# Kernel tuning notes

Hardware: AMD Instinct MI355X
Metric: run time of the kernel (lower is better)

## Reference

```python
import jax, jax.numpy as jnp
import numpy as np

B, S, D = 8, 2048, 512
EPS = 1e-6
ROPE_THETA = 10000.0


def setup_inputs() -> dict:
    key = jax.random.key(0)
    ks = jax.random.split(key, 8)
    scale = 0.02
    return {
        "x": jax.random.normal(ks[0], (B, S, D), dtype=jnp.float32),
        "conv_w": jax.random.normal(ks[1], (D, D, 3), dtype=jnp.float32) * scale,
        "conv_b": jnp.zeros((D,), dtype=jnp.float32),
        "pre_g": jnp.ones((D,), dtype=jnp.float32),
        "q_g": jnp.ones((D,), dtype=jnp.float32),
        "k_g": jnp.ones((D,), dtype=jnp.float32),
        "Wq": jax.random.normal(ks[2], (D, D), dtype=jnp.float32) * scale,
        "Wk": jax.random.normal(ks[3], (D, D), dtype=jnp.float32) * scale,
        "Wv": jax.random.normal(ks[4], (D, D), dtype=jnp.float32) * scale,
    }


def _rmsnorm(x, g, eps=EPS):
    ms = jnp.mean(jnp.square(x), axis=-1, keepdims=True)
    return x * jax.lax.rsqrt(ms + eps) * g


def _rope_tables(seq_len, head_dim, dtype=jnp.float32):
    inv = 1.0 / (ROPE_THETA ** (jnp.arange(0, head_dim, 2, dtype=dtype) / head_dim))
    freqs = jnp.arange(seq_len, dtype=dtype)[:, None] * inv[None, :]  # [S, D/2]
    return jnp.cos(freqs), jnp.sin(freqs)


def _apply_rope(x, cos, sin):
    # x: [B, S, D]; treat last dim as D/2 complex pairs (interleaved real/imag)
    b, s, d = x.shape
    xr = x.reshape(b, s, d // 2, 2)
    x0, x1 = xr[..., 0], xr[..., 1]
    c = cos[None, :, :]
    sn = sin[None, :, :]
    o0 = x0 * c - x1 * sn
    o1 = x0 * sn + x1 * c
    return jnp.stack([o0, o1], axis=-1).reshape(b, s, d)


def reference(x, conv_w, conv_b, pre_g, q_g, k_g, Wq, Wk, Wv):
    b, s, d = x.shape
    # Conv1d over sequence axis (kernel 3, padding 1)
    xc = jnp.transpose(x, (0, 2, 1))  # [B, D, S]
    xc = jax.lax.conv_general_dilated(
        xc, conv_w, window_strides=(1,), padding=[(1, 1)],
        dimension_numbers=("NCH", "OIH", "NCH"))
    xc = xc + conv_b[None, :, None]
    x_norm = _rmsnorm(jnp.transpose(xc, (0, 2, 1)), pre_g)  # [B, S, D]

    q = _rmsnorm(jnp.einsum("bsd,ed->bse", x_norm, Wq), q_g)
    k = _rmsnorm(jnp.einsum("bsd,ed->bse", x_norm, Wk), k_g)
    v = jnp.einsum("bsd,ed->bse", x_norm, Wv)

    cos, sin = _rope_tables(s, d, x.dtype)
    q = _apply_rope(q, cos, sin)
    k = _apply_rope(k, cos, sin)

    scores = jnp.einsum("bqd,bkd->bqk", q, k) / jnp.sqrt(jnp.asarray(d, x.dtype))
    w = jax.nn.softmax(scores, axis=-1)  # dropout is identity in eval mode
    attended = jnp.einsum("bqk,bkd->bqd", w, v)
    out = x + attended
    return out.mean(axis=1)  # [B, D]
```

## Files before the change

### kernel.cpp

```cpp
#include <hip/hip_runtime.h>
#include <math.h>

#define BB 8
#define SS 2048
#define SSG 2050
#define DDIM 512
#define KC 1536
#define EPSV 1e-6f
#define SCALE 0.044194173824159216f

typedef unsigned short ushort_t;
using short8 = __attribute__((ext_vector_type(8))) short;
using f32x4  = __attribute__((ext_vector_type(4))) float;

__device__ inline unsigned short f2bf(float f) {
    union { float f; unsigned int u; } v; v.f = f;
    unsigned int r = v.u + 0x7FFFu + ((v.u >> 16) & 1u);
    return (unsigned short)(r >> 16);
}
__device__ inline unsigned int packbf(float a, float b) {
    return (unsigned int)f2bf(a) | ((unsigned int)f2bf(b) << 16);
}
__device__ inline float bf2f(unsigned short s) {
    union { unsigned int u; float f; } v; v.u = ((unsigned int)s) << 16; return v.f;
}

__device__ inline void gload16(const ushort_t* g, ushort_t* l) {
    __builtin_amdgcn_global_load_lds(
        (__attribute__((address_space(1))) const void*)g,
        (__attribute__((address_space(3))) void*)l, 16, 0, 0);
}

__device__ inline short8 ldswz(const ushort_t* s, int row, int c) {
    return *reinterpret_cast<const short8*>(&s[(row << 6) + ((c ^ (row & 7)) << 3)]);
}

__device__ inline ushort_t* crow_ptr(ushort_t* As, ushort_t* Bs, int row) {
    return row < 64 ? As + row * 128 : Bs + (row - 64) * 128;
}

__global__ __launch_bounds__(256) void kx_cast(const float* __restrict__ x,
                                               ushort_t* __restrict__ xbf,
                                               float* __restrict__ xsum)
{
    const int t = threadIdx.x;
    const int b = blockIdx.y;
    const int r0 = blockIdx.x * 16;
    const int c0 = 2 * t;
    if (blockIdx.x == 0) {
        *reinterpret_cast<unsigned int*>(&xbf[((size_t)b * SSG) * DDIM + c0]) = 0u;
        *reinterpret_cast<unsigned int*>(&xbf[((size_t)b * SSG + SS + 1) * DDIM + c0]) = 0u;
    }
    float s0 = 0.f, s1 = 0.f;
    for (int r = 0; r < 16; r++) {
        size_t srow = (size_t)b * SS + r0 + r;
        size_t drow = (size_t)b * SSG + 1 + r0 + r;
        float2 v = *reinterpret_cast<const float2*>(&x[srow * DDIM + c0]);
        s0 += v.x; s1 += v.y;
        *reinterpret_cast<unsigned int*>(&xbf[drow * DDIM + c0]) = packbf(v.x, v.y);
    }
    atomicAdd(&xsum[b * DDIM + c0], s0);
    atomicAdd(&xsum[b * DDIM + c0 + 1], s1);
}

__global__ __launch_bounds__(256) void k0_prep(
    const float* __restrict__ conv_w, const float* __restrict__ Wq,
    const float* __restrict__ Wk, const float* __restrict__ Wv,
    ushort_t* __restrict__ wcat, ushort_t* __restrict__ wqkv)
{
    int idx = blockIdx.x * 256 + threadIdx.x;
    {
        int o = idx / KC, kk = idx - o * KC;
        int t = kk >> 9, i = kk & 511;
        wcat[idx] = f2bf(conv_w[(size_t)o * KC + i * 3 + t]);
    }
    {
        int n = idx >> 9, d = idx & 511;
        const float* src = (n < 512) ? &Wq[(size_t)n * DDIM + d]
                         : (n < 1024) ? &Wk[(size_t)(n - 512) * DDIM + d]
                         : &Wv[(size_t)(n - 1024) * DDIM + d];
        wqkv[idx] = f2bf(*src);
    }
}

__global__ __launch_bounds__(256) void ktab(float* __restrict__ rope)
{
    const int t = threadIdx.x;
    const int r0 = blockIdx.x * 8;
    const float invf = (float)pow(10000.0, -(double)(2 * t) / (double)DDIM);
    for (int r = 0; r < 8; r++) {
        int srow = r0 + r;
        float sn, cs;
        sincosf((float)srow * invf, &sn, &cs);
        *reinterpret_cast<float2*>(&rope[((size_t)srow << 9) + 2 * t]) = make_float2(cs, sn);
    }
}

#define COMPUTE_TILE(Acur, Bcur) do { \
    _Pragma("unroll") \
    for (int half = 0; half < 2; half++) { \
        const int cb = (half << 2) | lq; \
        short8 af0 = ldswz(Acur, wm * 64 +  0 + lm, cb); \
        short8 af1 = ldswz(Acur, wm * 64 + 16 + lm, cb); \
        short8 af2 = ldswz(Acur, wm * 64 + 32 + lm, cb); \
        short8 af3 = ldswz(Acur, wm * 64 + 48 + lm, cb); \
        _Pragma("unroll") \
        for (int nt = 0; nt < 4; nt++) { \
            short8 bfv = ldswz(Bcur, wn * 64 + nt * 16 + lm, cb); \
            acc[0][nt] = __builtin_amdgcn_mfma_f32_16x16x32_bf16(af0, bfv, acc[0][nt], 0, 0, 0); \
            acc[1][nt] = __builtin_amdgcn_mfma_f32_16x16x32_bf16(af1, bfv, acc[1][nt], 0, 0, 0); \
            acc[2][nt] = __builtin_amdgcn_mfma_f32_16x16x32_bf16(af2, bfv, acc[2][nt], 0, 0, 0); \
            acc[3][nt] = __builtin_amdgcn_mfma_f32_16x16x32_bf16(af3, bfv, acc[3][nt], 0, 0, 0); \
        } \
    } } while (0)

#define CSTORE_WIDE(GDSTROW, GPITCH) do { \
    const int row_l = t >> 1, half_ = t & 1, r7_ = row_l & 7; \
    const ushort_t* src_ = crow_ptr(As, Bs, row_l); \
    ushort_t* gdst_ = (GDSTROW); \
    _Pragma("unroll") \
    for (int i = 0; i < 8; i++) { \
        const int j = half_ * 8 + i; \
        *reinterpret_cast<short8*>(&gdst_[j * 8]) = \
            *reinterpret_cast<const short8*>(&src_[(j ^ r7_) << 3]); \
    } } while (0)

__global__ __launch_bounds__(256) void k1b_conv(
    const ushort_t* __restrict__ xbf, const ushort_t* __restrict__ wcat,
    const float* __restrict__ conv_b, ushort_t* __restrict__ ybf, float* __restrict__ rs)
{
    __shared__ alignas(16) ushort_t As[128 * 64];
    __shared__ alignas(16) ushort_t Bs[128 * 64];
    const int t = threadIdx.x;
    const int lane = t & 63, w = t >> 6;
    const int lm = lane & 15, lq = lane >> 4;
    const int wm = w >> 1, wn = w & 1;
    const int lr = lane >> 3;
    const int lc = ((lane & 7) ^ lr) << 3;
    const int s0 = blockIdx.x * 128;
    const int n0 = blockIdx.y * 128;
    const int b  = blockIdx.z;
    const ushort_t* Ag = xbf + (size_t)b * SSG * DDIM;
    const ushort_t* Bg = wcat + (size_t)n0 * KC;

    const ushort_t* pa[4]; const ushort_t* pb[4];
    int la[4];
    #pragma unroll
    for (int i = 0; i < 4; i++) {
        const int tr = (w * 4 + i) * 8 + lr;
        pa[i] = &Ag[(size_t)(s0 + tr) * DDIM + lc];
        pb[i] = &Bg[(size_t)tr * KC + lc];
        la[i] = (w * 4 + i) * 512;
    }

    f32x4 acc[4][4];
    #pragma unroll
    for (int i = 0; i < 4; i++)
        #pragma unroll
        for (int j = 0; j < 4; j++) acc[i][j] = (f32x4){0.f, 0.f, 0.f, 0.f};

    for (int dc = 0; dc < 24; dc++) {
        __syncthreads();
        const int koff = dc * 64;
        #pragma unroll
        for (int i = 0; i < 4; i++) {
            gload16(pa[i] + koff, &As[la[i]]);
            gload16(pb[i] + koff, &Bs[la[i]]);
        }
        __syncthreads();
        COMPUTE_TILE(As, Bs);
    }

    const int rbase = s0 + wm * 64;
    const int cbase = n0 + wn * 64;
    float* rsb = rs + (size_t)b * SS;
    float bias[4];
    #pragma unroll
    for (int nt = 0; nt < 4; nt++) bias[nt] = conv_b[cbase + nt * 16 + lm];
    __syncthreads();
    #pragma unroll
    for (int mt = 0; mt < 4; mt++) {
        #pragma unroll
        for (int r = 0; r < 4; r++) {
            const int rl = wm * 64 + mt * 16 + lq * 4 + r;
            ushort_t* lr_p = crow_ptr(As, Bs, rl);
            const int r7 = rl & 7;
            float pr = 0.f;
            #pragma unroll
            for (int nt = 0; nt < 4; nt++) {
                float val = acc[mt][nt][r] + bias[nt];
                const int c = wn * 64 + nt * 16 + lm;
                lr_p[(((c >> 3) ^ r7) << 3) | (c & 7)] = f2bf(val);
                pr = fmaf(val, val, pr);
            }
            pr += __shfl_xor(pr, 1, 64); pr += __shfl_xor(pr, 2, 64);
            pr += __shfl_xor(pr, 4, 64); pr += __shfl_xor(pr, 8, 64);
            if (lm == 0) atomicAdd(&rsb[rbase + mt * 16 + lq * 4 + r], pr);
        }
    }
    __syncthreads();
    ushort_t* yb = ybf + (size_t)b * SS * DDIM;
    CSTORE_WIDE(&yb[(size_t)(s0 + (t >> 1)) * DDIM + n0], DDIM);
}

__global__ __launch_bounds__(256) void k1n_norm(
    const ushort_t* __restrict__ ybf, const float* __restrict__ rs,
    const float* __restrict__ pre_g, ushort_t* __restrict__ xnbf)
{
    const int t = threadIdx.x;
    const int b = blockIdx.y;
    const int r0 = blockIdx.x * 8;
    float2 pg = *reinterpret_cast<const float2*>(&pre_g[2 * t]);
    for (int r = 0; r < 8; r++) {
        size_t row = (size_t)b * SS + r0 + r;
        float inv = rsqrtf(rs[row] * (1.0f / DDIM) + EPSV);
        unsigned int yv = *reinterpret_cast<const unsigned int*>(&ybf[row * DDIM + 2 * t]);
        float v0 = bf2f((ushort_t)(yv & 0xFFFF)), v1 = bf2f((ushort_t)(yv >> 16));
        *reinterpret_cast<unsigned int*>(&xnbf[row * DDIM + 2 * t]) =
            packbf(v0 * inv * pg.x, v1 * inv * pg.y);
    }
}

__global__ __launch_bounds__(256) void k1c_qkv(
    const ushort_t* __restrict__ xnbf, const ushort_t* __restrict__ wqkv,
    ushort_t* __restrict__ qraw, ushort_t* __restrict__ kraw, ushort_t* __restrict__ vb,
    float* __restrict__ rq, float* __restrict__ rk)
{
    __shared__ alignas(16) ushort_t As[128 * 64];
    __shared__ alignas(16) ushort_t Bs[128 * 64];
    const int t = threadIdx.x;
    const int lane = t & 63, w = t >> 6;
    const int lm = lane & 15, lq = lane >> 4;
    const int wm = w >> 1, wn = w & 1;
    const int lr = lane >> 3;
    const int lc = ((lane & 7) ^ lr) << 3;
    const int s0 = blockIdx.x * 128;
    const int n0 = blockIdx.y * 128;
    const int b  = blockIdx.z;
    const ushort_t* Ag = xnbf + ((size_t)b * SS + s0) * DDIM;
    const ushort_t* Bg = wqkv + (size_t)n0 * DDIM;

    const ushort_t* pa[4]; const ushort_t* pb[4];
    int la[4];
    #pragma unroll
    for (int i = 0; i < 4; i++) {
        const int tr = (w * 4 + i) * 8 + lr;
        pa[i] = &Ag[(size_t)tr * DDIM + lc];
        pb[i] = &Bg[(size_t)tr * DDIM + lc];
        la[i] = (w * 4 + i) * 512;
    }

    f32x4 acc[4][4];
    #pragma unroll
    for (int i = 0; i < 4; i++)
        #pragma unroll
        for (int j = 0; j < 4; j++) acc[i][j] = (f32x4){0.f, 0.f, 0.f, 0.f};

    for (int dc = 0; dc < 8; dc++) {
        __syncthreads();
        const int koff = dc * 64;
        #pragma unroll
        for (int i = 0; i < 4; i++) {
            gload16(pa[i] + koff, &As[la[i]]);
            gload16(pb[i] + koff, &Bs[la[i]]);
        }
        __syncthreads();
        COMPUTE_TILE(As, Bs);
    }

    const int which = blockIdx.y >> 2;
    const int rbase = s0 + wm * 64;
    const int gc0   = (blockIdx.y & 3) * 128;
    __syncthreads();
    if (which == 2) {
        #pragma unroll
        for (int mt = 0; mt < 4; mt++) {
            #pragma unroll
            for (int r = 0; r < 4; r++) {
                const int rl = wm * 64 + mt * 16 + lq * 4 + r;
                ushort_t* lr_p = crow_ptr(As, Bs, rl);
                const int r7 = rl & 7;
                #pragma unroll
                for (int nt = 0; nt < 4; nt++) {
                    const int c = wn * 64 + nt * 16 + lm;
                    lr_p[(((c >> 3) ^ r7) << 3) | (c & 7)] = f2bf(acc[mt][nt][r]);
                }
            }
        }
        __syncthreads();
        ushort_t* vbb = vb + (size_t)b * SS * DDIM;
        CSTORE_WIDE(&vbb[(size_t)(s0 + (t >> 1)) * DDIM + gc0], DDIM);
    } else {
        float* rb = (which ? rk : rq) + (size_t)b * SS;
        #pragma unroll
        for (int mt = 0; mt < 4; mt++) {
            #pragma unroll
            for (int r = 0; r < 4; r++) {
                const int rl = wm * 64 + mt * 16 + lq * 4 + r;
                ushort_t* lr_p = crow_ptr(As, Bs, rl);
                const int r7 = rl & 7;
                float pr = 0.f;
                #pragma unroll
                for (int nt = 0; nt < 4; nt++) {
                    float val = acc[mt][nt][r];
                    const int c = wn * 64 + nt * 16 + lm;
                    lr_p[(((c >> 3) ^ r7) << 3) | (c & 7)] = f2bf(val);
                    pr = fmaf(val, val, pr);
                }
                pr += __shfl_xor(pr, 1, 64); pr += __shfl_xor(pr, 2, 64);
                pr += __shfl_xor(pr, 4, 64); pr += __shfl_xor(pr, 8, 64);
                if (lm == 0) atomicAdd(&rb[rbase + mt * 16 + lq * 4 + r], pr);
            }
        }
        __syncthreads();
        ushort_t* db2 = (which ? kraw : qraw) + (size_t)b * SS * DDIM;
        CSTORE_WIDE(&db2[(size_t)(s0 + (t >> 1)) * DDIM + gc0], DDIM);
    }
}

__global__ __launch_bounds__(256) void k1d_rope(
    ushort_t* q_io, ushort_t* k_io,
    const float* __restrict__ rq, const float* __restrict__ rk,
    const float* __restrict__ q_g, const float* __restrict__ k_g,
    const float* __restrict__ rope)
{
    const int t = threadIdx.x;
    const int b = blockIdx.y;
    const int r0 = blockIdx.x * 8;
    const int c0 = 2 * t;
    float qg0 = q_g[c0], qg1 = q_g[c0 + 1];
    float kg0 = k_g[c0], kg1 = k_g[c0 + 1];
    for (int r = 0; r < 8; r++) {
        int srow = r0 + r;
        size_t rowi = (size_t)b * SS + srow;
        float iq = rsqrtf(rq[rowi] * (1.0f / DDIM) + EPSV);
        float ik = rsqrtf(rk[rowi] * (1.0f / DDIM) + EPSV);
        size_t off = rowi * DDIM + c0;
        unsigned int qv = *reinterpret_cast<const unsigned int*>(&q_io[off]);
        unsigned int kv = *reinterpret_cast<const unsigned int*>(&k_io[off]);
        float q0 = bf2f((ushort_t)(qv & 0xFFFF)) * iq * qg0;
        float q1 = bf2f((ushort_t)(qv >> 16)) * iq * qg1;
        float k0v = bf2f((ushort_t)(kv & 0xFFFF)) * ik * kg0;
        float k1v = bf2f((ushort_t)(kv >> 16)) * ik * kg1;
        float2 cs2 = *reinterpret_cast<const float2*>(&rope[((size_t)srow << 9) + c0]);
        float cs = cs2.x, sn = cs2.y;
        *reinterpret_cast<unsigned int*>(&q_io[off]) = packbf(q0 * cs - q1 * sn, q0 * sn + q1 * cs);
        *reinterpret_cast<unsigned int*>(&k_io[off]) = packbf(k0v * cs - k1v * sn, k0v * sn + k1v * cs);
    }
}

__global__ __launch_bounds__(256) void k2a_rowsum(
    const ushort_t* __restrict__ qb, const ushort_t* __restrict__ kb,
    ushort_t* __restrict__ P, float* __restrict__ l)
{
    __shared__ alignas(16) ushort_t As[128 * 64];
    __shared__ alignas(16) ushort_t Bs[128 * 64];
    const int t = threadIdx.x;
    const int lane = t & 63, w = t >> 6;
    const int lm = lane & 15, lq = lane >> 4;
    const int wm = w >> 1, wn = w & 1;
    const int lr = lane >> 3;
    const int lc = ((lane & 7) ^ lr) << 3;
    const int b  = blockIdx.x;
    const int qt = blockIdx.y;
    const int kt = blockIdx.z;
    const ushort_t* Ag = qb + ((size_t)b * SS + qt * 128) * DDIM;
    const ushort_t* Bg = kb + ((size_t)b * SS + kt * 128) * DDIM;

    const ushort_t* pa[4]; const ushort_t* pb[4];
    int la[4];
    #pragma unroll
    for (int i = 0; i < 4; i++) {
        const int tr = (w * 4 + i) * 8 + lr;
        pa[i] = &Ag[(size_t)tr * DDIM + lc];
        pb[i] = &Bg[(size_t)tr * DDIM + lc];
        la[i] = (w * 4 + i) * 512;
    }

    f32x4 acc[4][4];
    #pragma unroll
    for (int i = 0; i < 4; i++)
        #pragma unroll
        for (int j = 0; j < 4; j++) acc[i][j] = (f32x4){0.f, 0.f, 0.f, 0.f};

    for (int dc = 0; dc < 8; dc++) {
        __syncthreads();
        const int koff = dc * 64;
        #pragma unroll
        for (int i = 0; i < 4; i++) {
            gload16(pa[i] + koff, &As[la[i]]);
            gload16(pb[i] + koff, &Bs[la[i]]);
        }
        __syncthreads();
        COMPUTE_TILE(As, Bs);
    }

    float* lrow = l + (size_t)b * SS + qt * 128;
    __syncthreads();
    #pragma unroll
    for (int mt = 0; mt < 4; mt++) {
        #pragma unroll
        for (int r = 0; r < 4; r++) {
            const int rl = wm * 64 + mt * 16 + lq * 4 + r;
            ushort_t* lr_p = crow_ptr(As, Bs, rl);
            const int r7 = rl & 7;
            float rowp = 0.f;
            #pragma unroll
            for (int nt = 0; nt < 4; nt++) {
                float e = __expf(acc[mt][nt][r] * SCALE);
                const int c = wn * 64 + nt * 16 + lm;
                lr_p[(((c >> 3) ^ r7) << 3) | (c & 7)] = f2bf(e);
                rowp += e;
            }
            rowp += __shfl_xor(rowp, 1, 64); rowp += __shfl_xor(rowp, 2, 64);
            rowp += __shfl_xor(rowp, 4, 64); rowp += __shfl_xor(rowp, 8, 64);
            if (lm == 0) atomicAdd(&lrow[rl], rowp);
        }
    }
    __syncthreads();
    ushort_t* Pb = P + (size_t)b * SS * SS;
    CSTORE_WIDE(&Pb[(size_t)(qt * 128 + (t >> 1)) * SS + kt * 128], SS);
}

__global__ __launch_bounds__(256) void k2c_colred(
    const ushort_t* __restrict__ P, const float* __restrict__ l,
    float* __restrict__ cw)
{
    const int t = threadIdx.x;
    const int b = blockIdx.z;
    const int k0 = blockIdx.x * 1024 + t * 4;
    const int q0 = blockIdx.y * 128;
    const ushort_t* Pb = P + ((size_t)b * SS + q0) * SS;
    const float* lb = l + (size_t)b * SS + q0;
    float a0 = 0.f, a1 = 0.f, a2 = 0.f, a3 = 0.f;
    for (int q = 0; q < 128; q++) {
        float rl = 1.0f / lb[q];
        uint2 pp = *reinterpret_cast<const uint2*>(&Pb[(size_t)q * SS + k0]);
        a0 = fmaf(bf2f((ushort_t)(pp.x & 0xFFFF)), rl, a0);
        a1 = fmaf(bf2f((ushort_t)(pp.x >> 16)), rl, a1);
        a2 = fmaf(bf2f((ushort_t)(pp.y & 0xFFFF)), rl, a2);
        a3 = fmaf(bf2f((ushort_t)(pp.y >> 16)), rl, a3);
    }
    atomicAdd(&cw[(size_t)b * SS + k0], a0);
    atomicAdd(&cw[(size_t)b * SS + k0 + 1], a1);
    atomicAdd(&cw[(size_t)b * SS + k0 + 2], a2);
    atomicAdd(&cw[(size_t)b * SS + k0 + 3], a3);
}

__global__ __launch_bounds__(256) void k4_out(
    const float* __restrict__ xsum, const ushort_t* __restrict__ v,
    const float* __restrict__ cwv, float* __restrict__ out)
{
    const int b = blockIdx.x, c = blockIdx.y;
    const int t = threadIdx.x;
    const int srow0 = c * (SS / 16);
    const ushort_t* vb = v + ((size_t)b * SS + srow0) * DDIM;
    const float* cwb   = cwv + (size_t)b * SS + srow0;
    float a0 = (c == 0) ? xsum[b * DDIM + t]       : 0.f;
    float a1 = (c == 0) ? xsum[b * DDIM + t + 256] : 0.f;
    for (int r = 0; r < SS / 16; r++) {
        float w = cwb[r];
        a0 += w * bf2f(vb[(size_t)r * DDIM + t]);
        a1 += w * bf2f(vb[(size_t)r * DDIM + t + 256]);
    }
    atomicAdd(&out[b * DDIM + t],       a0 * (1.0f / SS));
    atomicAdd(&out[b * DDIM + t + 256], a1 * (1.0f / SS));
}

extern "C" void kernel_launch(void* const* d_in, const int* in_sizes, int n_in,
                              void* d_out, int out_size, void* d_ws, size_t ws_size,
                              hipStream_t stream)
{
    const float* x      = (const float*)d_in[0];
    const float* conv_w = (const float*)d_in[1];
    const float* conv_b = (const float*)d_in[2];
    const float* pre_g  = (const float*)d_in[3];
    const float* q_g    = (const float*)d_in[4];
    const float* k_g    = (const float*)d_in[5];
    const float* Wq     = (const float*)d_in[6];
    const float* Wk     = (const float*)d_in[7];
    const float* Wv     = (const float*)d_in[8];
    float* out          = (float*)d_out;

    const size_t NTOK  = (size_t)BB * SS * DDIM;
    const size_t NTOKG = (size_t)BB * SSG * DDIM;
    char* p = (char*)d_ws;
    ushort_t* xbf = (ushort_t*)p; p += NTOKG * 2;
    ushort_t* ybf = (ushort_t*)p; p += NTOK * 2;
    ushort_t* xn  = (ushort_t*)p; p += NTOK * 2;
    char* padreg = p;             p += NTOK * 2;
    ushort_t* qio = (ushort_t*)p; p += NTOK * 2;
    ushort_t* kio = (ushort_t*)p; p += NTOK * 2;
    ushort_t* vb  = (ushort_t*)p; p += NTOK * 2;
    ushort_t* wcat = (ushort_t*)p; p += (size_t)DDIM * KC * 2;
    ushort_t* wqkv = (ushort_t*)p; p += (size_t)KC * DDIM * 2;
    float* rs   = (float*)p; p += (size_t)BB * SS * 4;
    float* rq   = (float*)p; p += (size_t)BB * SS * 4;
    float* rk   = (float*)p; p += (size_t)BB * SS * 4;
    float* lbuf = (float*)p; p += (size_t)BB * SS * 4;
    float* cwb  = (float*)p; p += (size_t)BB * SS * 4;
    float* xsum = (float*)p; p += (size_t)BB * DDIM * 4;

    ushort_t* Pbuf = xbf;
    float* rope = (float*)padreg;

    (void)hipMemsetAsync(d_out, 0, (size_t)out_size * sizeof(float), stream);
    (void)hipMemsetAsync(rs, 0, ((size_t)BB * SS * 5 + (size_t)BB * DDIM) * sizeof(float), stream);

    kx_cast<<<dim3(SS / 16, BB), 256, 0, stream>>>(x, xbf, xsum);
    k0_prep<<<dim3(DDIM * KC / 256), 256, 0, stream>>>(conv_w, Wq, Wk, Wv, wcat, wqkv);
    ktab<<<dim3(SS / 8), 256, 0, stream>>>(rope);
    k1b_conv<<<dim3(SS / 128, 4, BB), 256, 0, stream>>>(xbf, wcat, conv_b, ybf, rs);
    k1n_norm<<<dim3(SS / 8, BB), 256, 0, stream>>>(ybf, rs, pre_g, xn);
    k1c_qkv<<<dim3(SS / 128, 12, BB), 256, 0, stream>>>(xn, wqkv, qio, kio, vb, rq, rk);
    k1d_rope<<<dim3(SS / 8, BB), 256, 0, stream>>>(qio, kio, rq, rk, q_g, k_g, rope);
    k2a_rowsum<<<dim3(BB, SS / 128, SS / 128), 256, 0, stream>>>(qio, kio, Pbuf, lbuf);
    k2c_colred<<<dim3(SS / 1024, SS / 128, BB), 256, 0, stream>>>(Pbuf, lbuf, cwb);
    k4_out<<<dim3(BB, 16), 256, 0, stream>>>(xsum, vb, cwb, out);
}
```

Baseline: 314.4 us.

## Store GEMM epilogues directly to global and put batch index on blockIdx.x

Drops the LDS-staged, swizzled epilogue with its extra barriers in the conv, QKV and score kernels. Each lane now writes its bf16 accumulator elements straight to global memory, and the row sums are reduced per row. Separately, every launch grid is reordered so the batch index is the fastest-varying block dimension, which changes block scheduling and cache locality. The cost is narrow 2-byte scattered global stores in place of 16-byte coalesced rows, which may hurt store efficiency, especially for the large P matrix.

New measurement: 275.6 us. 12.4% less time.

```diff
diff --git a/kernel.cpp b/kernel.cpp
--- a/kernel.cpp
+++ b/kernel.cpp
@@ -35,19 +35,15 @@
     return *reinterpret_cast<const short8*>(&s[(row << 6) + ((c ^ (row & 7)) << 3)]);
 }
 
-__device__ inline ushort_t* crow_ptr(ushort_t* As, ushort_t* Bs, int row) {
-    return row < 64 ? As + row * 128 : Bs + (row - 64) * 128;
-}
-
 __global__ __launch_bounds__(256) void kx_cast(const float* __restrict__ x,
                                                ushort_t* __restrict__ xbf,
                                                float* __restrict__ xsum)
 {
     const int t = threadIdx.x;
-    const int b = blockIdx.y;
-    const int r0 = blockIdx.x * 16;
+    const int b = blockIdx.x;
+    const int r0 = blockIdx.y * 16;
     const int c0 = 2 * t;
-    if (blockIdx.x == 0) {
+    if (blockIdx.y == 0) {
         *reinterpret_cast<unsigned int*>(&xbf[((size_t)b * SSG) * DDIM + c0]) = 0u;
         *reinterpret_cast<unsigned int*>(&xbf[((size_t)b * SSG + SS + 1) * DDIM + c0]) = 0u;
     }
@@ -114,17 +110,6 @@
         } \
     } } while (0)
 
-#define CSTORE_WIDE(GDSTROW, GPITCH) do { \
-    const int row_l = t >> 1, half_ = t & 1, r7_ = row_l & 7; \
-    const ushort_t* src_ = crow_ptr(As, Bs, row_l); \
-    ushort_t* gdst_ = (GDSTROW); \
-    _Pragma("unroll") \
-    for (int i = 0; i < 8; i++) { \
-        const int j = half_ * 8 + i; \
-        *reinterpret_cast<short8*>(&gdst_[j * 8]) = \
-            *reinterpret_cast<const short8*>(&src_[(j ^ r7_) << 3]); \
-    } } while (0)
-
 __global__ __launch_bounds__(256) void k1b_conv(
     const ushort_t* __restrict__ xbf, const ushort_t* __restrict__ wcat,
     const float* __restrict__ conv_b, ushort_t* __restrict__ ybf, float* __restrict__ rs)
@@ -137,9 +122,9 @@
     const int wm = w >> 1, wn = w & 1;
     const int lr = lane >> 3;
     const int lc = ((lane & 7) ^ lr) << 3;
-    const int s0 = blockIdx.x * 128;
-    const int n0 = blockIdx.y * 128;
-    const int b  = blockIdx.z;
+    const int b  = blockIdx.x;
+    const int s0 = blockIdx.y * 128;
+    const int n0 = blockIdx.z * 128;
     const ushort_t* Ag = xbf + (size_t)b * SSG * DDIM;
     const ushort_t* Bg = wcat + (size_t)n0 * KC;
 
@@ -173,34 +158,31 @@
 
     const int rbase = s0 + wm * 64;
     const int cbase = n0 + wn * 64;
+    ushort_t* yb = ybf + (size_t)b * SS * DDIM;
     float* rsb = rs + (size_t)b * SS;
     float bias[4];
     #pragma unroll
     for (int nt = 0; nt < 4; nt++) bias[nt] = conv_b[cbase + nt * 16 + lm];
-    __syncthreads();
     #pragma unroll
     for (int mt = 0; mt < 4; mt++) {
+        float pr[4] = {0.f, 0.f, 0.f, 0.f};
+        #pragma unroll
+        for (int nt = 0; nt < 4; nt++) {
+            #pragma unroll
+            for (int r = 0; r < 4; r++) {
+                float val = acc[mt][nt][r] + bias[nt];
+                yb[(size_t)(rbase + mt * 16 + lq * 4 + r) * DDIM + cbase + nt * 16 + lm] = f2bf(val);
+                pr[r] = fmaf(val, val, pr[r]);
+            }
+        }
         #pragma unroll
         for (int r = 0; r < 4; r++) {
-            const int rl = wm * 64 + mt * 16 + lq * 4 + r;
-            ushort_t* lr_p = crow_ptr(As, Bs, rl);
-            const int r7 = rl & 7;
-            float pr = 0.f;
-            #pragma unroll
-            for (int nt = 0; nt < 4; nt++) {
-                float val = acc[mt][nt][r] + bias[nt];
-                const int c = wn * 64 + nt * 16 + lm;
-                lr_p[(((c >> 3) ^ r7) << 3) | (c & 7)] = f2bf(val);
-                pr = fmaf(val, val, pr);
-            }
-            pr += __shfl_xor(pr, 1, 64); pr += __shfl_xor(pr, 2, 64);
-            pr += __shfl_xor(pr, 4, 64); pr += __shfl_xor(pr, 8, 64);
-            if (lm == 0) atomicAdd(&rsb[rbase + mt * 16 + lq * 4 + r], pr);
-        }
-    }
-    __syncthreads();
-    ushort_t* yb = ybf + (size_t)b * SS * DDIM;
-    CSTORE_WIDE(&yb[(size_t)(s0 + (t >> 1)) * DDIM + n0], DDIM);
+            float p = pr[r];
+            p += __shfl_xor(p, 1, 64); p += __shfl_xor(p, 2, 64);
+            p += __shfl_xor(p, 4, 64); p += __shfl_xor(p, 8, 64);
+            if (lm == 0) atomicAdd(&rsb[rbase + mt * 16 + lq * 4 + r], p);
+        }
+    }
 }
 
 __global__ __launch_bounds__(256) void k1n_norm(
@@ -208,8 +190,8 @@
     const float* __restrict__ pre_g, ushort_t* __restrict__ xnbf)
 {
     const int t = threadIdx.x;
-    const int b = blockIdx.y;
-    const int r0 = blockIdx.x * 8;
+    const int b = blockIdx.x;
+    const int r0 = blockIdx.y * 8;
     float2 pg = *reinterpret_cast<const float2*>(&pre_g[2 * t]);
     for (int r = 0; r < 8; r++) {
         size_t row = (size_t)b * SS + r0 + r;
@@ -234,9 +216,10 @@
     const int wm = w >> 1, wn = w & 1;
     const int lr = lane >> 3;
     const int lc = ((lane & 7) ^ lr) << 3;
-    const int s0 = blockIdx.x * 128;
-    const int n0 = blockIdx.y * 128;
-    const int b  = blockIdx.z;
+    const int b  = blockIdx.x;
+    const int s0 = blockIdx.y * 128;
+    const int nt9 = blockIdx.z;
+    const int n0 = nt9 * 128;
     const ushort_t* Ag = xnbf + ((size_t)b * SS + s0) * DDIM;
     const ushort_t* Bg = wqkv + (size_t)n0 * DDIM;
 
@@ -268,53 +251,42 @@
         COMPUTE_TILE(As, Bs);
     }
 
-    const int which = blockIdx.y >> 2;
+    const int which = nt9 >> 2;
     const int rbase = s0 + wm * 64;
-    const int gc0   = (blockIdx.y & 3) * 128;
-    __syncthreads();
+    const int cbase = ((nt9 & 3) * 128) + wn * 64;
     if (which == 2) {
+        ushort_t* vbb = vb + (size_t)b * SS * DDIM;
+        #pragma unroll
+        for (int mt = 0; mt < 4; mt++)
+            #pragma unroll
+            for (int nt = 0; nt < 4; nt++)
+                #pragma unroll
+                for (int r = 0; r < 4; r++)
+                    vbb[(size_t)(rbase + mt * 16 + lq * 4 + r) * DDIM + cbase + nt * 16 + lm] =
+                        f2bf(acc[mt][nt][r]);
+    } else {
+        ushort_t* db2 = (which ? kraw : qraw) + (size_t)b * SS * DDIM;
+        float* rb = (which ? rk : rq) + (size_t)b * SS;
         #pragma unroll
         for (int mt = 0; mt < 4; mt++) {
+            float pr[4] = {0.f, 0.f, 0.f, 0.f};
+            #pragma unroll
+            for (int nt = 0; nt < 4; nt++) {
+                #pragma unroll
+                for (int r = 0; r < 4; r++) {
+                    float val = acc[mt][nt][r];
+                    db2[(size_t)(rbase + mt * 16 + lq * 4 + r) * DDIM + cbase + nt * 16 + lm] = f2bf(val);
+                    pr[r] = fmaf(val, val, pr[r]);
+                }
+            }
             #pragma unroll
             for (int r = 0; r < 4; r++) {
-                const int rl = wm * 64 + mt * 16 + lq * 4 + r;
-                ushort_t* lr_p = crow_ptr(As, Bs, rl);
-                const int r7 = rl & 7;
-                #pragma unroll
-                for (int nt = 0; nt < 4; nt++) {
-                    const int c = wn * 64 + nt * 16 + lm;
-                    lr_p[(((c >> 3) ^ r7) << 3) | (c & 7)] = f2bf(acc[mt][nt][r]);
-                }
+                float p = pr[r];
+                p += __shfl_xor(p, 1, 64); p += __shfl_xor(p, 2, 64);
+                p += __shfl_xor(p, 4, 64); p += __shfl_xor(p, 8, 64);
+                if (lm == 0) atomicAdd(&rb[rbase + mt * 16 + lq * 4 + r], p);
             }
         }
-        __syncthreads();
-        ushort_t* vbb = vb + (size_t)b * SS * DDIM;
-        CSTORE_WIDE(&vbb[(size_t)(s0 + (t >> 1)) * DDIM + gc0], DDIM);
-    } else {
-        float* rb = (which ? rk : rq) + (size_t)b * SS;
-        #pragma unroll
-        for (int mt = 0; mt < 4; mt++) {
-            #pragma unroll
-            for (int r = 0; r < 4; r++) {
-                const int rl = wm * 64 + mt * 16 + lq * 4 + r;
-                ushort_t* lr_p = crow_ptr(As, Bs, rl);
-                const int r7 = rl & 7;
-                float pr = 0.f;
-                #pragma unroll
-                for (int nt = 0; nt < 4; nt++) {
-                    float val = acc[mt][nt][r];
-                    const int c = wn * 64 + nt * 16 + lm;
-                    lr_p[(((c >> 3) ^ r7) << 3) | (c & 7)] = f2bf(val);
-                    pr = fmaf(val, val, pr);
-                }
-                pr += __shfl_xor(pr, 1, 64); pr += __shfl_xor(pr, 2, 64);
-                pr += __shfl_xor(pr, 4, 64); pr += __shfl_xor(pr, 8, 64);
-                if (lm == 0) atomicAdd(&rb[rbase + mt * 16 + lq * 4 + r], pr);
-            }
-        }
-        __syncthreads();
-        ushort_t* db2 = (which ? kraw : qraw) + (size_t)b * SS * DDIM;
-        CSTORE_WIDE(&db2[(size_t)(s0 + (t >> 1)) * DDIM + gc0], DDIM);
     }
 }
 
@@ -325,8 +297,8 @@
     const float* __restrict__ rope)
 {
     const int t = threadIdx.x;
-    const int b = blockIdx.y;
-    const int r0 = blockIdx.x * 8;
+    const int b = blockIdx.x;
+    const int r0 = blockIdx.y * 8;
     const int c0 = 2 * t;
     float qg0 = q_g[c0], qg1 = q_g[c0 + 1];
     float kg0 = k_g[c0], kg1 = k_g[c0 + 1];
@@ -395,31 +367,28 @@
         COMPUTE_TILE(As, Bs);
     }
 
-    float* lrow = l + (size_t)b * SS + qt * 128;
-    __syncthreads();
+    const int rbase = qt * 128 + wm * 64;
+    const int cbase = kt * 128 + wn * 64;
+    ushort_t* Pb = P + (size_t)b * SS * SS;
+    float* lrow = l + (size_t)b * SS;
     #pragma unroll
     for (int mt = 0; mt < 4; mt++) {
         #pragma unroll
         for (int r = 0; r < 4; r++) {
-            const int rl = wm * 64 + mt * 16 + lq * 4 + r;
-            ushort_t* lr_p = crow_ptr(As, Bs, rl);
-            const int r7 = rl & 7;
+            const int row = rbase + mt * 16 + lq * 4 + r;
             float rowp = 0.f;
             #pragma unroll
             for (int nt = 0; nt < 4; nt++) {
                 float e = __expf(acc[mt][nt][r] * SCALE);
-                const int c = wn * 64 + nt * 16 + lm;
-                lr_p[(((c >> 3) ^ r7) << 3) | (c & 7)] = f2bf(e);
+                Pb[(size_t)row * SS + cbase + nt * 16 + lm] = f2bf(e);
                 rowp += e;
             }
-            rowp += __shfl_xor(rowp, 1, 64); rowp += __shfl_xor(rowp, 2, 64);
-            rowp += __shfl_xor(rowp, 4, 64); rowp += __shfl_xor(rowp, 8, 64);
-            if (lm == 0) atomicAdd(&lrow[rl], rowp);
-        }
-    }
-    __syncthreads();
-    ushort_t* Pb = P + (size_t)b * SS * SS;
-    CSTORE_WIDE(&Pb[(size_t)(qt * 128 + (t >> 1)) * SS + kt * 128], SS);
+            float p = rowp;
+            p += __shfl_xor(p, 1, 64); p += __shfl_xor(p, 2, 64);
+            p += __shfl_xor(p, 4, 64); p += __shfl_xor(p, 8, 64);
+            if (lm == 0) atomicAdd(&lrow[row], p);
+        }
+    }
 }
 
 __global__ __launch_bounds__(256) void k2c_colred(
@@ -427,9 +396,9 @@
     float* __restrict__ cw)
 {
     const int t = threadIdx.x;
-    const int b = blockIdx.z;
-    const int k0 = blockIdx.x * 1024 + t * 4;
+    const int b = blockIdx.x;
     const int q0 = blockIdx.y * 128;
+    const int k0 = blockIdx.z * 1024 + t * 4;
     const ushort_t* Pb = P + ((size_t)b * SS + q0) * SS;
     const float* lb = l + (size_t)b * SS + q0;
     float a0 = 0.f, a1 = 0.f, a2 = 0.f, a3 = 0.f;
@@ -507,14 +476,14 @@
     (void)hipMemsetAsync(d_out, 0, (size_t)out_size * sizeof(float), stream);
     (void)hipMemsetAsync(rs, 0, ((size_t)BB * SS * 5 + (size_t)BB * DDIM) * sizeof(float), stream);
 
-    kx_cast<<<dim3(SS / 16, BB), 256, 0, stream>>>(x, xbf, xsum);
+    kx_cast<<<dim3(BB, SS / 16), 256, 0, stream>>>(x, xbf, xsum);
     k0_prep<<<dim3(DDIM * KC / 256), 256, 0, stream>>>(conv_w, Wq, Wk, Wv, wcat, wqkv);
     ktab<<<dim3(SS / 8), 256, 0, stream>>>(rope);
-    k1b_conv<<<dim3(SS / 128, 4, BB), 256, 0, stream>>>(xbf, wcat, conv_b, ybf, rs);
-    k1n_norm<<<dim3(SS / 8, BB), 256, 0, stream>>>(ybf, rs, pre_g, xn);
-    k1c_qkv<<<dim3(SS / 128, 12, BB), 256, 0, stream>>>(xn, wqkv, qio, kio, vb, rq, rk);
-    k1d_rope<<<dim3(SS / 8, BB), 256, 0, stream>>>(qio, kio, rq, rk, q_g, k_g, rope);
+    k1b_conv<<<dim3(BB, SS / 128, 4), 256, 0, stream>>>(xbf, wcat, conv_b, ybf, rs);
+    k1n_norm<<<dim3(BB, SS / 8), 256, 0, stream>>>(ybf, rs, pre_g, xn);
+    k1c_qkv<<<dim3(BB, SS / 128, 12), 256, 0, stream>>>(xn, wqkv, qio, kio, vb, rq, rk);
+    k1d_rope<<<dim3(BB, SS / 8), 256, 0, stream>>>(qio, kio, rq, rk, q_g, k_g, rope);
     k2a_rowsum<<<dim3(BB, SS / 128, SS / 128), 256, 0, stream>>>(qio, kio, Pbuf, lbuf);
-    k2c_colred<<<dim3(SS / 1024, SS / 128, BB), 256, 0, stream>>>(Pbuf, lbuf, cwb);
+    k2c_colred<<<dim3(BB, SS / 128, SS / 1024), 256, 0, stream>>>(Pbuf, lbuf, cwb);
     k4_out<<<dim3(BB, 16), 256, 0, stream>>>(xsum, vb, cwb, out);
 }
```
